# Kernel tuning notes

Measured on AMD Instinct MI355X. Metric: run time of the kernel, lower is better.

Reference implementation:

```python
import jax, jax.numpy as jnp
import numpy as np

B, V, C, H, W, D = 1, 3, 32, 320, 320, 32


def setup_inputs() -> dict:
    key = jax.random.key(0)
    ks = jax.random.split(key, 14)
    feats = jax.random.normal(ks[0], (B, V, C, H, W), jnp.float32)
    # Valid pinhole projections: P = [[K @ [R|t]], [0,0,0,1]], identity rotation,
    # horizontal baselines sized so the warp stays mostly in-image over the depth range.
    K = np.array([[400.0, 0.0, W / 2.0], [0.0, 400.0, H / 2.0], [0.0, 0.0, 1.0]])
    mats = []
    for tx in (0.0, 100.0, -100.0):
        Rt = np.eye(4)
        Rt[0, 3] = tx
        P = np.eye(4)
        P[:3, :4] = K @ Rt[:3, :4]
        mats.append(P)
    proj = jnp.asarray(np.broadcast_to(np.stack(mats)[None], (B, V, 4, 4)).copy(), jnp.float32)
    planes = jnp.linspace(425.0, 935.0, D, dtype=jnp.float32)
    depth_values = jnp.broadcast_to(planes[None, :, None, None], (B, D, H, W)).astype(jnp.float32)
    s = 0.05  # small init so exp(reg_cost) stays well-scaled
    W0 = s * jax.random.normal(ks[1], (8, C, 3, 3), jnp.float32)
    Ws1 = s * jax.random.normal(ks[2], (8, 8, 3, 3), jnp.float32)
    W1 = s * jax.random.normal(ks[3], (16, 8, 3, 3), jnp.float32)
    Ws2 = s * jax.random.normal(ks[4], (16, 16, 3, 3), jnp.float32)
    W2 = s * jax.random.normal(ks[5], (32, 16, 3, 3), jnp.float32)
    Ws3 = s * jax.random.normal(ks[6], (32, 32, 3, 3), jnp.float32)
    W3 = s * jax.random.normal(ks[7], (64, 32, 3, 3), jnp.float32)
    Ws4 = s * jax.random.normal(ks[8], (64, 64, 3, 3), jnp.float32)
    U4 = s * jax.random.normal(ks[9], (32, 64, 1, 1), jnp.float32)
    U3 = s * jax.random.normal(ks[10], (16, 32, 1, 1), jnp.float32)
    U2 = s * jax.random.normal(ks[11], (8, 16, 1, 1), jnp.float32)
    Wout = s * jax.random.normal(ks[12], (1, 8, 3, 3), jnp.float32)
    return dict(feats=feats, proj=proj, depth_values=depth_values, W0=W0, Ws1=Ws1,
                W1=W1, Ws2=Ws2, W2=W2, Ws3=Ws3, W3=W3, Ws4=Ws4, U4=U4, U3=U3, U2=U2, Wout=Wout)


def _conv(x, w, stride=1):
    return jax.lax.conv_general_dilated(x, w, (stride, stride), 'SAME',
                                        dimension_numbers=('NCHW', 'OIHW', 'NCHW'))


def _up2(x):
    return jnp.repeat(jnp.repeat(x, 2, axis=2), 2, axis=3)


def _bilinear(img, x, y):
    # img [C,H,W]; x,y [N] pixel coords; zero padding, align_corners semantics
    Cc, Hh, Ww = img.shape
    x0 = jnp.floor(x)
    y0 = jnp.floor(y)
    wx = x - x0
    wy = y - y0

    def tap(xi, yi):
        valid = ((xi >= 0) & (xi <= Ww - 1) & (yi >= 0) & (yi <= Hh - 1)).astype(img.dtype)
        xc = jnp.clip(xi, 0, Ww - 1).astype(jnp.int32)
        yc = jnp.clip(yi, 0, Hh - 1).astype(jnp.int32)
        return img[:, yc, xc] * valid  # [C,N]

    return (tap(x0, y0) * (1 - wx) * (1 - wy) + tap(x0 + 1, y0) * wx * (1 - wy)
            + tap(x0, y0 + 1) * (1 - wx) * wy + tap(x0 + 1, y0 + 1) * wx * wy)


def _forward(feats, proj, depth_values, W0, Ws1, W1, Ws2, W2, Ws3, W3, Ws4, U4, U3, U2, Wout):
    Bn, Vn, Cn, Hn, Wn = feats.shape
    Dn = depth_values.shape[1]
    N = Hn * Wn
    relu = jax.nn.relu
    ref = feats[:, 0]
    ref_sq = ref * ref
    # Precompute per-src-view rotated pixel rays and translations.
    inv_ref = jnp.linalg.inv(proj[:, 0])                       # [B,4,4]
    rel = jnp.einsum('bvij,bjk->bvik', proj[:, 1:], inv_ref)   # [B,V-1,4,4]
    rot, trans = rel[:, :, :3, :3], rel[:, :, :3, 3]
    ys, xs = jnp.meshgrid(jnp.arange(Hn), jnp.arange(Wn), indexing='ij')
    pix = jnp.stack([xs.ravel(), ys.ravel(), jnp.ones(N)], 0).astype(feats.dtype)  # [3,N]
    rot_pix = jnp.einsum('bvij,jn->bvin', rot, pix)            # [B,V-1,3,N]

    def regularize(x, s1, s2, s3, s4):
        c1 = relu(_conv(x, W0) + _conv(s1, Ws1))
        c2 = relu(_conv(c1, W1, 2) + _conv(s2, Ws2))
        c3 = relu(_conv(c2, W2, 2) + _conv(s3, Ws3))
        c4 = relu(_conv(c3, W3, 2) + _conv(s4, Ws4))
        u3 = c3 + _up2(_conv(c4, U4))
        u2 = c2 + _up2(_conv(u3, U3))
        u1 = c1 + _up2(_conv(u2, U2))
        return _conv(u1, Wout), c1, c2, c3, c4

    def step(carry, depth_slice):  # depth_slice [B,H,W]
        s1, s2, s3, s4, exp_sum, depth_img, max_prob = carry
        vol_sum, vol_sq = ref, ref_sq
        dflat = depth_slice.reshape(Bn, 1, N)
        for v in range(Vn - 1):
            xyz = rot_pix[:, v] * dflat + trans[:, v, :, None]   # [B,3,N]
            px = xyz[:, 0] / xyz[:, 2]
            py = xyz[:, 1] / xyz[:, 2]
            warped = jax.vmap(_bilinear)(feats[:, v + 1], px, py).reshape(Bn, Cn, Hn, Wn)
            vol_sum = vol_sum + warped
            vol_sq = vol_sq + warped * warped
        variance = vol_sq / Vn - (vol_sum / Vn) ** 2
        cost, s1, s2, s3, s4 = regularize(variance, s1, s2, s3, s4)
        prob = jnp.exp(cost)                                     # [B,1,H,W]
        max_prob = jnp.maximum(max_prob, prob)                   # == flag*prob + (1-flag)*max
        depth_img = depth_img + depth_slice[:, None] * prob
        exp_sum = exp_sum + prob
        return (s1, s2, s3, s4, exp_sum, depth_img, max_prob), None

    z = lambda c, h, w: jnp.zeros((Bn, c, h, w), feats.dtype)
    init = (z(8, Hn, Wn), z(16, Hn // 2, Wn // 2), z(32, Hn // 4, Wn // 4), z(64, Hn // 8, Wn // 8),
            z(1, Hn, Wn), z(1, Hn, Wn), z(1, Hn, Wn))
    carry, _ = jax.lax.scan(step, init, jnp.moveaxis(depth_values, 1, 0))
    _, _, _, _, exp_sum, depth_img, max_prob = carry
    es = exp_sum + 1e-10
    depth_map = (depth_img / es)[:, 0]
    prob_map = (max_prob / es)[:, 0]
    return jnp.stack([depth_map, prob_map], axis=1)  # [B,2,H,W]


def reference(feats, proj, depth_values, W0, Ws1, W1, Ws2, W2, Ws3, W3, Ws4, U4, U3, U2, Wout):
    return _forward(feats, proj, depth_values, W0, Ws1, W1, Ws2, W2, Ws3, W3, Ws4, U4, U3, U2, Wout)
```

## Files before the change

### kernel.cpp

```cpp
#include <hip/hip_runtime.h>
#include <hip/hip_bf16.h>
#include <hip/hip_fp16.h>
#include <math.h>

#define HH 320
#define WW 320
#define NP (HH*WW)
#define CC 32
#define DD 32
#define H2 160
#define W2 160
#define N2 (H2*W2)
#define H4 80
#define W4 80
#define N4 (H4*W4)
#define H8 40
#define W8 40
#define N8 (H8*W8)

#define AHW 18
#define AHH 10
#define ANH (AHW*AHH)
#define ABUF_STRIDE 184

#define U3_NPX 24
#define U3_ST  25
#define U2_NPX 60
#define U2_ST  61
#define U1_NPX 180
#define U1_ST  181

#define SMEM_FLOATS (32*U3_ST + 16*U2_ST + 8*U1_ST)

#define C1SZ (8*NP)
#define C2SZ (16*N2)
#define C3SZ (32*N4)
#define C4SZ (64*N8)

#define OFF_REL  0
#define FH_FLOATS (3*CC*NP/2)
#define OFF_FH   64
#define OFF_C1R  (OFF_FH + FH_FLOATS)
#define OFF_C2R  (OFF_C1R + 5*C1SZ)
#define OFF_C3R  (OFF_C2R + 4*C2SZ)
#define OFF_C4R  (OFF_C3R + 3*C3SZ)
#define OFF_ESUM (OFF_C4R + 2*C4SZ)
#define OFF_DIMG (OFF_ESUM + NP)
#define OFF_MAXP (OFF_DIMG + NP)
#define OFF_END  (OFF_MAXP + NP)

#define D_BEG 0
#define C_BEG 128
#define B_BEG 352
#define A_BEG 752
#define U_BEG 1552
#define TOT_BLK 2352

__global__ void k_prep(const float* __restrict__ proj, float* __restrict__ rel) {
    if (threadIdx.x != 0 || blockIdx.x != 0) return;
    double a[4][8];
    for (int i = 0; i < 4; i++)
        for (int j = 0; j < 4; j++) {
            a[i][j] = (double)proj[i*4 + j];
            a[i][j+4] = (i == j) ? 1.0 : 0.0;
        }
    for (int c = 0; c < 4; c++) {
        int pv = c; double best = fabs(a[c][c]);
        for (int r = c+1; r < 4; r++) {
            double v = fabs(a[r][c]);
            if (v > best) { best = v; pv = r; }
        }
        if (pv != c)
            for (int j = 0; j < 8; j++) { double t = a[c][j]; a[c][j] = a[pv][j]; a[pv][j] = t; }
        double inv = 1.0 / a[c][c];
        for (int j = 0; j < 8; j++) a[c][j] *= inv;
        for (int r = 0; r < 4; r++) if (r != c) {
            double f = a[r][c];
            for (int j = 0; j < 8; j++) a[r][j] -= f * a[c][j];
        }
    }
    for (int v = 1; v < 3; v++) {
        const float* P = proj + v*16;
        double rm[4][4];
        for (int i = 0; i < 4; i++)
            for (int j = 0; j < 4; j++) {
                double s = 0.0;
                for (int k = 0; k < 4; k++) s += (double)P[i*4 + k] * a[k][j+4];
                rm[i][j] = s;
            }
        float* o = rel + (v-1)*12;
        o[0]=(float)rm[0][0]; o[1]=(float)rm[0][1]; o[2]=(float)rm[0][2];
        o[3]=(float)rm[1][0]; o[4]=(float)rm[1][1]; o[5]=(float)rm[1][2];
        o[6]=(float)rm[2][0]; o[7]=(float)rm[2][1]; o[8]=(float)rm[2][2];
        o[9]=(float)rm[0][3]; o[10]=(float)rm[1][3]; o[11]=(float)rm[2][3];
    }
}

__global__ __launch_bounds__(256) void k_tofp16(const float* __restrict__ feats,
                                                __half* __restrict__ fh) {
    int i = blockIdx.x*256 + threadIdx.x;
    int base = i*8;
    if (base >= 3*CC*NP) return;
    float4 a = *(const float4*)(feats + base);
    float4 b = *(const float4*)(feats + base + 4);
    __half h[8];
    h[0]=__float2half(a.x); h[1]=__float2half(a.y); h[2]=__float2half(a.z); h[3]=__float2half(a.w);
    h[4]=__float2half(b.x); h[5]=__float2half(b.y); h[6]=__float2half(b.z); h[7]=__float2half(b.w);
    *(float4*)(fh + base) = *(float4*)h;
}


__device__ void stageA(int blk, int d,
        const __half* __restrict__ fh, const float* __restrict__ rel,
        const float* __restrict__ depthv, float* __restrict__ c1r,
        const float* __restrict__ W0, const float* __restrict__ Ws1,
        float* buf) {
    const float* s1 = c1r + (size_t)((d+4)%5)*C1SZ;
    float* c1out = c1r + (size_t)(d%5)*C1SZ;
    int bx = blk % 20, by = blk / 20;
    int ox0 = bx*16, oy0 = by*8;
    int tid = threadIdx.x;

    int ppix[2]; bool inimg[2];
    int rb[2][4];
    float cf[2][8];
#pragma unroll
    for (int j = 0; j < 2; j++) {
        int hp = tid + j*128;
        inimg[j] = false; ppix[j] = 0;
#pragma unroll
        for (int q = 0; q < 4; q++) rb[j][q] = 0;
#pragma unroll
        for (int q = 0; q < 8; q++) cf[j][q] = 0.0f;
        if (hp < ANH) {
            int hy = hp / AHW, hx = hp - hy*AHW;
            int gy = oy0 + hy - 1, gx = ox0 + hx - 1;
            if (gy >= 0 && gy < HH && gx >= 0 && gx < WW) {
                inimg[j] = true;
                int p = gy*WW + gx; ppix[j] = p;
                float depth = depthv[(size_t)d*NP + p];
                float fx = (float)gx, fy = (float)gy;
#pragma unroll
                for (int v = 0; v < 2; v++) {
                    const float* r = rel + v*12;
                    float X = (r[0]*fx + r[1]*fy + r[2]) * depth + r[9];
                    float Y = (r[3]*fx + r[4]*fy + r[5]) * depth + r[10];
                    float Z = (r[6]*fx + r[7]*fy + r[8]) * depth + r[11];
                    float iz = 1.0f / Z;
                    float px = fminf(fmaxf(X*iz, -2.0f), (float)(WW+1));
                    float py = fminf(fmaxf(Y*iz, -2.0f), (float)(HH+1));
                    float x0f = floorf(px), y0f = floorf(py);
                    float wx = px - x0f, wy = py - y0f;
                    int x0 = (int)x0f, y0 = (int)y0f;
                    int xb = min(max(x0, 0), WW-2);
                    float cA, cB;
                    if (x0 >= 0 && x0 <= WW-2)      { cA = 1.0f-wx; cB = wx; }
                    else if (x0 == -1)              { cA = wx;      cB = 0.0f; }
                    else if (x0 == WW-1)            { cA = 0.0f;    cB = 1.0f-wx; }
                    else                            { cA = 0.0f;    cB = 0.0f; }
#pragma unroll
                    for (int rr = 0; rr < 2; rr++) {
                        int yr = y0 + rr;
                        float wyr = rr ? wy : 1.0f-wy;
                        bool vy = (yr >= 0) && (yr < HH);
                        int yrc = min(max(yr, 0), HH-1);
                        rb[j][v*2+rr] = yrc*WW + xb;
                        cf[j][v*4+rr*2+0] = vy ? wyr*cA : 0.0f;
                        cf[j][v*4+rr*2+1] = vy ? wyr*cB : 0.0f;
                    }
                }
            }
        }
    }

    int opx = tid & 15, opy = tid >> 4;
    float acc[8];
#pragma unroll
    for (int o = 0; o < 8; o++) acc[o] = 0.0f;
    const float inv3 = 1.0f/3.0f;

    for (int chunk = 0; chunk < 4; chunk++) {
        int c0 = chunk*8;
#pragma unroll
        for (int j = 0; j < 2; j++) {
            int hp = tid + j*128;
            if (hp < ANH) {
                if (!inimg[j]) {
#pragma unroll
                    for (int c = 0; c < 8; c++) buf[c*ABUF_STRIDE + hp] = 0.0f;
                } else {
                    int p = ppix[j];
#pragma unroll
                    for (int c = 0; c < 8; c++) {
                        int cg = c0 + c;
                        float rv = __half2float(fh[(size_t)cg*NP + p]);
                        const __half* p1 = fh + (size_t)(CC + cg)*NP;
                        float t1 = cf[j][0]*__half2float(p1[rb[j][0]])
                                 + cf[j][1]*__half2float(p1[rb[j][0]+1])
                                 + cf[j][2]*__half2float(p1[rb[j][1]])
                                 + cf[j][3]*__half2float(p1[rb[j][1]+1]);
                        const __half* p2 = fh + (size_t)(2*CC + cg)*NP;
                        float t2 = cf[j][4]*__half2float(p2[rb[j][2]])
                                 + cf[j][5]*__half2float(p2[rb[j][2]+1])
                                 + cf[j][6]*__half2float(p2[rb[j][3]])
                                 + cf[j][7]*__half2float(p2[rb[j][3]+1]);
                        float sum = rv + t1 + t2;
                        float sq  = rv*rv + t1*t1 + t2*t2;
                        float m = sum*inv3;
                        buf[c*ABUF_STRIDE + hp] = sq*inv3 - m*m;
                    }
                }
            }
        }
        __syncthreads();
        for (int ci = 0; ci < 8; ci++) {
            float t[9];
#pragma unroll
            for (int ky = 0; ky < 3; ky++)
#pragma unroll
                for (int kx = 0; kx < 3; kx++)
                    t[ky*3+kx] = buf[ci*ABUF_STRIDE + (opy+ky)*AHW + opx + kx];
#pragma unroll
            for (int o = 0; o < 8; o++) {
                const float* w = W0 + (o*32 + c0 + ci)*9;
                float a = acc[o];
#pragma unroll
                for (int k = 0; k < 9; k++) a += t[k]*w[k];
                acc[o] = a;
            }
        }
        __syncthreads();
    }

#pragma unroll
    for (int j = 0; j < 2; j++) {
        int hp = tid + j*128;
        if (hp < ANH) {
#pragma unroll
            for (int c = 0; c < 8; c++)
                buf[c*ABUF_STRIDE + hp] = inimg[j] ? s1[(size_t)c*NP + ppix[j]] : 0.0f;
        }
    }
    __syncthreads();
    for (int ci = 0; ci < 8; ci++) {
        float t[9];
#pragma unroll
        for (int ky = 0; ky < 3; ky++)
#pragma unroll
            for (int kx = 0; kx < 3; kx++)
                t[ky*3+kx] = buf[ci*ABUF_STRIDE + (opy+ky)*AHW + opx + kx];
#pragma unroll
        for (int o = 0; o < 8; o++) {
            const float* w = Ws1 + (o*8 + ci)*9;
            float a = acc[o];
#pragma unroll
            for (int k = 0; k < 9; k++) a += t[k]*w[k];
            acc[o] = a;
        }
    }
    int outp = (oy0 + opy)*WW + ox0 + opx;
#pragma unroll
    for (int o = 0; o < 8; o++) c1out[(size_t)o*NP + outp] = fmaxf(acc[o], 0.0f);
}

__device__ void stageB(int chunk, int og, int d,
        const float* __restrict__ c1r, float* __restrict__ c2r,
        const float* __restrict__ W1, const float* __restrict__ Ws2) {
    const float* c1 = c1r + (size_t)(d%5)*C1SZ;
    const float* s2 = c2r + (size_t)((d+3)%4)*C2SZ;
    float* c2 = c2r + (size_t)(d%4)*C2SZ;
    int p = chunk*128 + threadIdx.x;
    int y = p / W2, x = p - y*W2;
    int offsA[9]; float mskA[9];
#pragma unroll
    for (int k = 0; k < 9; k++) {
        int yy = 2*y + k/3, xx = 2*x + k%3;
        bool v = (yy < HH) && (xx < WW);
        offsA[k] = v ? yy*WW + xx : 0;
        mskA[k] = v ? 1.0f : 0.0f;
    }
    int offsB[9]; float mskB[9];
#pragma unroll
    for (int k = 0; k < 9; k++) {
        int yy = y + k/3 - 1, xx = x + k%3 - 1;
        bool v = (yy >= 0) && (yy < H2) && (xx >= 0) && (xx < W2);
        offsB[k] = v ? yy*W2 + xx : 0;
        mskB[k] = v ? 1.0f : 0.0f;
    }
    float acc[8];
#pragma unroll
    for (int o = 0; o < 8; o++) acc[o] = 0.0f;
    for (int ci = 0; ci < 8; ci++) {
        const float* b = c1 + (size_t)ci*NP;
        float t[9];
#pragma unroll
        for (int k = 0; k < 9; k++) t[k] = b[offsA[k]] * mskA[k];
#pragma unroll
        for (int o = 0; o < 8; o++) {
            const float* w = W1 + ((og*8 + o)*8 + ci)*9;
            float a = acc[o];
#pragma unroll
            for (int k = 0; k < 9; k++) a += t[k]*w[k];
            acc[o] = a;
        }
    }
    for (int ci = 0; ci < 16; ci++) {
        const float* b = s2 + (size_t)ci*N2;
        float t[9];
#pragma unroll
        for (int k = 0; k < 9; k++) t[k] = b[offsB[k]] * mskB[k];
#pragma unroll
        for (int o = 0; o < 8; o++) {
            const float* w = Ws2 + ((og*8 + o)*16 + ci)*9;
            float a = acc[o];
#pragma unroll
            for (int k = 0; k < 9; k++) a += t[k]*w[k];
            acc[o] = a;
        }
    }
#pragma unroll
    for (int o = 0; o < 8; o++) c2[(size_t)(og*8 + o)*N2 + p] = fmaxf(acc[o], 0.0f);
}

__device__ void stageC(int chunk, int og, int d,
        const float* __restrict__ c2r, float* __restrict__ c3r,
        const float* __restrict__ W2w, const float* __restrict__ Ws3) {
    const float* c2 = c2r + (size_t)(d%4)*C2SZ;
    const float* s3 = c3r + (size_t)((d+2)%3)*C3SZ;
    float* c3 = c3r + (size_t)(d%3)*C3SZ;
    int p = chunk*128 + threadIdx.x;
    int y = p / W4, x = p - y*W4;
    int offsA[9]; float mskA[9];
#pragma unroll
    for (int k = 0; k < 9; k++) {
        int yy = 2*y + k/3, xx = 2*x + k%3;
        bool v = (yy < H2) && (xx < W2);
        offsA[k] = v ? yy*W2 + xx : 0;
        mskA[k] = v ? 1.0f : 0.0f;
    }
    int offsB[9]; float mskB[9];
#pragma unroll
    for (int k = 0; k < 9; k++) {
        int yy = y + k/3 - 1, xx = x + k%3 - 1;
        bool v = (yy >= 0) && (yy < H4) && (xx >= 0) && (xx < W4);
        offsB[k] = v ? yy*W4 + xx : 0;
        mskB[k] = v ? 1.0f : 0.0f;
    }
    float acc[8];
#pragma unroll
    for (int o = 0; o < 8; o++) acc[o] = 0.0f;
    for (int ci = 0; ci < 16; ci++) {
        const float* b = c2 + (size_t)ci*N2;
        float t[9];
#pragma unroll
        for (int k = 0; k < 9; k++) t[k] = b[offsA[k]] * mskA[k];
#pragma unroll
        for (int o = 0; o < 8; o++) {
            const float* w = W2w + ((og*8 + o)*16 + ci)*9;
            float a = acc[o];
#pragma unroll
            for (int k = 0; k < 9; k++) a += t[k]*w[k];
            acc[o] = a;
        }
    }
    for (int ci = 0; ci < 32; ci++) {
        const float* b = s3 + (size_t)ci*N4;
        float t[9];
#pragma unroll
        for (int k = 0; k < 9; k++) t[k] = b[offsB[k]] * mskB[k];
#pragma unroll
        for (int o = 0; o < 8; o++) {
            const float* w = Ws3 + ((og*8 + o)*32 + ci)*9;
            float a = acc[o];
#pragma unroll
            for (int k = 0; k < 9; k++) a += t[k]*w[k];
            acc[o] = a;
        }
    }
#pragma unroll
    for (int o = 0; o < 8; o++) c3[(size_t)(og*8 + o)*N4 + p] = fmaxf(acc[o], 0.0f);
}

__device__ void stageD(int chunk, int og, int d,
        const float* __restrict__ c3r, float* __restrict__ c4r,
        const float* __restrict__ W3w, const float* __restrict__ Ws4) {
    const float* c3 = c3r + (size_t)(d%3)*C3SZ;
    const float* s4 = c4r + (size_t)((d+1)%2)*C4SZ;
    float* c4 = c4r + (size_t)(d%2)*C4SZ;
    int p = chunk*128 + threadIdx.x;
    if (p >= N8) return;
    int y = p / W8, x = p - y*W8;
    int offsA[9]; float mskA[9];
#pragma unroll
    for (int k = 0; k < 9; k++) {
        int yy = 2*y + k/3, xx = 2*x + k%3;
        bool v = (yy < H4) && (xx < W4);
        offsA[k] = v ? yy*W4 + xx : 0;
        mskA[k] = v ? 1.0f : 0.0f;
    }
    int offsB[9]; float mskB[9];
#pragma unroll
    for (int k = 0; k < 9; k++) {
        int yy = y + k/3 - 1, xx = x + k%3 - 1;
        bool v = (yy >= 0) && (yy < H8) && (xx >= 0) && (xx < W8);
        offsB[k] = v ? yy*W8 + xx : 0;
        mskB[k] = v ? 1.0f : 0.0f;
    }
    float acc[8];
#pragma unroll
    for (int o = 0; o < 8; o++) acc[o] = 0.0f;
    for (int ci = 0; ci < 32; ci++) {
        const float* b = c3 + (size_t)ci*N4;
        float t[9];
#pragma unroll
        for (int k = 0; k < 9; k++) t[k] = b[offsA[k]] * mskA[k];
#pragma unroll
        for (int o = 0; o < 8; o++) {
            const float* w = W3w + ((og*8 + o)*32 + ci)*9;
            float a = acc[o];
#pragma unroll
            for (int k = 0; k < 9; k++) a += t[k]*w[k];
            acc[o] = a;
        }
    }
    for (int ci = 0; ci < 64; ci++) {
        const float* b = s4 + (size_t)ci*N8;
        float t[9];
#pragma unroll
        for (int k = 0; k < 9; k++) t[k] = b[offsB[k]] * mskB[k];
#pragma unroll
        for (int o = 0; o < 8; o++) {
            const float* w = Ws4 + ((og*8 + o)*64 + ci)*9;
            float a = acc[o];
#pragma unroll
            for (int k = 0; k < 9; k++) a += t[k]*w[k];
            acc[o] = a;
        }
    }
#pragma unroll
    for (int o = 0; o < 8; o++) c4[(size_t)(og*8 + o)*N8 + p] = fmaxf(acc[o], 0.0f);
}

__device__ void stageU(int blk, int d,
        const float* __restrict__ c1r, const float* __restrict__ c2r,
        const float* __restrict__ c3r, const float* __restrict__ c4r,
        const float* __restrict__ U4, const float* __restrict__ U3w,
        const float* __restrict__ U2w, const float* __restrict__ Wout,
        const float* __restrict__ depthv,
        float* __restrict__ esum, float* __restrict__ dimg,
        float* __restrict__ maxp, float* smem) {
    const float* c1 = c1r + (size_t)(d%5)*C1SZ;
    const float* c2 = c2r + (size_t)(d%4)*C2SZ;
    const float* c3 = c3r + (size_t)(d%3)*C3SZ;
    const float* c4 = c4r + (size_t)(d%2)*C4SZ;
    const float* dsl = depthv + (size_t)d*NP;
    float* u3s = smem;
    float* u2s = smem + 32*U3_ST;
    float* u1s = u2s + 16*U2_ST;
    int bx = blk % 20, by = blk / 20;
    int x0 = bx*16, y0 = by*8;
    int qx0 = (x0>>2) - 1, qy0 = (y0>>2) - 1;
    int hx0 = (x0>>1) - 1, hy0 = (y0>>1) - 1;
    int tid = threadIdx.x;

    for (int i = tid; i < 32*U3_NPX; i += 128) {
        int ch = i / U3_NPX, pp = i - ch*U3_NPX;
        int y4 = qy0 + pp/6, x4 = qx0 + pp%6;
        int y4c = min(max(y4,0),H4-1), x4c = min(max(x4,0),W4-1);
        int pl = (y4c>>1)*W8 + (x4c>>1);
        const float* w = U4 + ch*64;
        float s = c3[(size_t)ch*N4 + y4c*W4 + x4c];
#pragma unroll 8
        for (int ci = 0; ci < 64; ci++) s += c4[(size_t)ci*N8 + pl]*w[ci];
        u3s[ch*U3_ST + pp] = s;
    }
    __syncthreads();
    for (int i = tid; i < 16*U2_NPX; i += 128) {
        int ch = i / U2_NPX, pp = i - ch*U2_NPX;
        int y2 = hy0 + pp/10, x2 = hx0 + pp%10;
        int y2c = min(max(y2,0),H2-1), x2c = min(max(x2,0),W2-1);
        int ly = (y2c>>1)-qy0, lx = (x2c>>1)-qx0;
        const float* w = U3w + ch*32;
        float s = c2[(size_t)ch*N2 + y2c*W2 + x2c];
#pragma unroll 8
        for (int ci = 0; ci < 32; ci++) s += u3s[ci*U3_ST + ly*6 + lx]*w[ci];
        u2s[ch*U2_ST + pp] = s;
    }
    __syncthreads();
    for (int i = tid; i < 8*U1_NPX; i += 128) {
        int ch = i / U1_NPX, pp = i - ch*U1_NPX;
        int gy = y0 + pp/AHW - 1, gx = x0 + pp%AHW - 1;
        float s = 0.0f;
        if (gy >= 0 && gy < HH && gx >= 0 && gx < WW) {
            int ly = (gy>>1)-hy0, lx = (gx>>1)-hx0;
            const float* w = U2w + ch*16;
            s = c1[(size_t)ch*NP + gy*WW + gx];
#pragma unroll
            for (int ci = 0; ci < 16; ci++) s += u2s[ci*U2_ST + ly*10 + lx]*w[ci];
        }
        u1s[ch*U1_ST + pp] = s;
    }
    __syncthreads();
    int opx = tid & 15, opy = tid >> 4;
    int base = opy*AHW + opx;
    float cost = 0.0f;
#pragma unroll
    for (int ci = 0; ci < 8; ci++) {
        const float* w = Wout + ci*9;
#pragma unroll
        for (int ky = 0; ky < 3; ky++)
#pragma unroll
            for (int kx = 0; kx < 3; kx++)
                cost += u1s[ci*U1_ST + base + ky*AHW + kx]*w[ky*3+kx];
    }
    int p = (y0+opy)*WW + x0 + opx;
    float prob = expf(cost);
    esum[p] += prob;
    dimg[p] += dsl[p]*prob;
    maxp[p] = fmaxf(maxp[p], prob);
}

__global__ __launch_bounds__(128) void k_uber(
        int t,
        const __half* __restrict__ fh, const float* __restrict__ rel,
        const float* __restrict__ depthv,
        const float* __restrict__ W0, const float* __restrict__ Ws1,
        const float* __restrict__ W1, const float* __restrict__ Ws2,
        const float* __restrict__ W2w, const float* __restrict__ Ws3,
        const float* __restrict__ W3w, const float* __restrict__ Ws4,
        const float* __restrict__ U4, const float* __restrict__ U3,
        const float* __restrict__ U2, const float* __restrict__ Wout,
        float* __restrict__ c1r, float* __restrict__ c2r,
        float* __restrict__ c3r, float* __restrict__ c4r,
        float* __restrict__ esum, float* __restrict__ dimg,
        float* __restrict__ maxp) {
    __shared__ float smem[SMEM_FLOATS];
    int b = blockIdx.x;
    if (b < C_BEG) {
        int d = t - 3;
        int og = b / 16, chunk = b % 16;
        if (d >= 0 && d < DD && chunk < 13) stageD(chunk, og, d, c3r, c4r, W3w, Ws4);
    } else if (b < B_BEG) {
        int d = t - 2;
        int local = b - C_BEG;
        int og = local / 56, chunk = local % 56;
        if (d >= 0 && d < DD && chunk < 50) stageC(chunk, og, d, c2r, c3r, W2w, Ws3);
    } else if (b < A_BEG) {
        int d = t - 1;
        int local = b - B_BEG;
        int og = local / 200, chunk = local % 200;
        if (d >= 0 && d < DD) stageB(chunk, og, d, c1r, c2r, W1, Ws2);
    } else if (b < U_BEG) {
        int d = t;
        if (d < DD) stageA(b - A_BEG, d, fh, rel, depthv, c1r, W0, Ws1, smem);
    } else {
        int d = t - 4;
        if (d >= 0 && d < DD)
            stageU(b - U_BEG, d, c1r, c2r, c3r, c4r, U4, U3, U2, Wout, depthv,
                   esum, dimg, maxp, smem);
    }
}

__global__ __launch_bounds__(256) void k_final(
        const float* __restrict__ exp_sum, const float* __restrict__ depth_img,
        const float* __restrict__ max_prob, float* __restrict__ out) {
    int p = blockIdx.x*256 + threadIdx.x;
    if (p >= NP) return;
    float es = exp_sum[p] + 1e-10f;
    out[p] = depth_img[p] / es;
    out[NP + p] = max_prob[p] / es;
}

extern "C" void kernel_launch(void* const* d_in, const int* in_sizes, int n_in,
                              void* d_out, int out_size, void* d_ws, size_t ws_size,
                              hipStream_t stream) {
    const float* feats = (const float*)d_in[0];
    const float* proj  = (const float*)d_in[1];
    const float* depthv= (const float*)d_in[2];
    const float* W0  = (const float*)d_in[3];
    const float* Ws1 = (const float*)d_in[4];
    const float* W1  = (const float*)d_in[5];
    const float* Ws2 = (const float*)d_in[6];
    const float* W2w = (const float*)d_in[7];
    const float* Ws3 = (const float*)d_in[8];
    const float* W3w = (const float*)d_in[9];
    const float* Ws4 = (const float*)d_in[10];
    const float* U4  = (const float*)d_in[11];
    const float* U3  = (const float*)d_in[12];
    const float* U2  = (const float*)d_in[13];
    const float* Wout= (const float*)d_in[14];

    float* ws = (float*)d_ws;
    float* rel  = ws + OFF_REL;
    __half* fh  = (__half*)(ws + OFF_FH);
    float* c1r  = ws + OFF_C1R;
    float* c2r  = ws + OFF_C2R;
    float* c3r  = ws + OFF_C3R;
    float* c4r  = ws + OFF_C4R;
    float* esum = ws + OFF_ESUM;
    float* dimg = ws + OFF_DIMG;
    float* maxp = ws + OFF_MAXP;

    hipMemsetAsync(c1r, 0, (size_t)(OFF_END - OFF_C1R) * sizeof(float), stream);
    k_prep<<<1, 1, 0, stream>>>(proj, rel);
    k_tofp16<<<dim3(3*CC*NP/8/256), 256, 0, stream>>>(feats, fh);

    for (int t = 0; t < DD + 4; t++) {
        k_uber<<<dim3(TOT_BLK), 128, 0, stream>>>(t, fh, rel, depthv,
            W0, Ws1, W1, Ws2, W2w, Ws3, W3w, Ws4, U4, U3, U2, Wout,
            c1r, c2r, c3r, c4r, esum, dimg, maxp);
    }
    k_final<<<dim3(400), 256, 0, stream>>>(esum, dimg, maxp, (float*)d_out);
}
```

Baseline: 3.125 ms.

## Switch fp16 features to pixel-major layout and double uber-kernel block size

The fp16 feature copy now uses a channel-last layout with 32 halves per pixel. Stage A's bilinear gathers become 16-byte vector loads of 8 channels instead of scalar strided half loads, and stage A splits its 8 output channels across two 128-thread halves. Blocks are raised to 256 threads: stages B/C/D cover 256 pixels per block and stage U covers a 16x16 tile, so block counts per stage are recomputed. This aims to cut gather transactions and the number of blocks. The cost is a strided transpose in the conversion kernel and more shared memory per block.

```diff
diff --git a/kernel.cpp b/kernel.cpp
--- a/kernel.cpp
+++ b/kernel.cpp
@@ -19,18 +19,13 @@
 #define N8 (H8*W8)
 
 #define AHW 18
-#define AHH 10
-#define ANH (AHW*AHH)
+#define ANH (AHW*10)
 #define ABUF_STRIDE 184
 
-#define U3_NPX 24
-#define U3_ST  25
-#define U2_NPX 60
-#define U2_ST  61
-#define U1_NPX 180
-#define U1_ST  181
-
-#define SMEM_FLOATS (32*U3_ST + 16*U2_ST + 8*U1_ST)
+#define U3S 37
+#define U2S 101
+#define U1S 325
+#define SMEM_FLOATS (32*U3S + 16*U2S + 8*U1S)
 
 #define C1SZ (8*NP)
 #define C2SZ (16*N2)
@@ -38,7 +33,7 @@
 #define C4SZ (64*N8)
 
 #define OFF_REL  0
-#define FH_FLOATS (3*CC*NP/2)
+#define FH_FLOATS (3*NP*CC/2)
 #define OFF_FH   64
 #define OFF_C1R  (OFF_FH + FH_FLOATS)
 #define OFF_C2R  (OFF_C1R + 5*C1SZ)
@@ -50,11 +45,18 @@
 #define OFF_END  (OFF_MAXP + NP)
 
 #define D_BEG 0
-#define C_BEG 128
-#define B_BEG 352
-#define A_BEG 752
-#define U_BEG 1552
-#define TOT_BLK 2352
+#define C_BEG 64
+#define B_BEG 192
+#define A_BEG 400
+#define U_BEG 1200
+#define TOT_BLK 1600
+
+__device__ __forceinline__ void load8h(const __half* b, float o[8]) {
+    float4 f = *reinterpret_cast<const float4*>(b);
+    const __half2* h = reinterpret_cast<const __half2*>(&f);
+#pragma unroll
+    for (int j = 0; j < 4; j++) { float2 t = __half22float2(h[j]); o[2*j] = t.x; o[2*j+1] = t.y; }
+}
 
 __global__ void k_prep(const float* __restrict__ proj, float* __restrict__ rel) {
     if (threadIdx.x != 0 || blockIdx.x != 0) return;
@@ -99,14 +101,15 @@
 __global__ __launch_bounds__(256) void k_tofp16(const float* __restrict__ feats,
                                                 __half* __restrict__ fh) {
     int i = blockIdx.x*256 + threadIdx.x;
-    int base = i*8;
-    if (base >= 3*CC*NP) return;
-    float4 a = *(const float4*)(feats + base);
-    float4 b = *(const float4*)(feats + base + 4);
-    __half h[8];
-    h[0]=__float2half(a.x); h[1]=__float2half(a.y); h[2]=__float2half(a.z); h[3]=__float2half(a.w);
-    h[4]=__float2half(b.x); h[5]=__float2half(b.y); h[6]=__float2half(b.z); h[7]=__float2half(b.w);
-    *(float4*)(fh + base) = *(float4*)h;
+    if (i >= 3*NP) return;
+    int v = i / NP, p = i - v*NP;
+    const float* src = feats + (size_t)v*CC*NP + p;
+    union { __half h[32]; float4 f4[4]; } u;
+#pragma unroll
+    for (int c = 0; c < 32; c++) u.h[c] = __float2half(src[(size_t)c*NP]);
+    float4* dst = (float4*)(fh + (size_t)i*32);
+#pragma unroll
+    for (int q = 0; q < 4; q++) dst[q] = u.f4[q];
 }
 
 
@@ -121,94 +124,87 @@
     int ox0 = bx*16, oy0 = by*8;
     int tid = threadIdx.x;
 
-    int ppix[2]; bool inimg[2];
-    int rb[2][4];
-    float cf[2][8];
-#pragma unroll
-    for (int j = 0; j < 2; j++) {
-        int hp = tid + j*128;
-        inimg[j] = false; ppix[j] = 0;
-#pragma unroll
-        for (int q = 0; q < 4; q++) rb[j][q] = 0;
-#pragma unroll
-        for (int q = 0; q < 8; q++) cf[j][q] = 0.0f;
-        if (hp < ANH) {
-            int hy = hp / AHW, hx = hp - hy*AHW;
-            int gy = oy0 + hy - 1, gx = ox0 + hx - 1;
-            if (gy >= 0 && gy < HH && gx >= 0 && gx < WW) {
-                inimg[j] = true;
-                int p = gy*WW + gx; ppix[j] = p;
-                float depth = depthv[(size_t)d*NP + p];
-                float fx = (float)gx, fy = (float)gy;
-#pragma unroll
-                for (int v = 0; v < 2; v++) {
-                    const float* r = rel + v*12;
-                    float X = (r[0]*fx + r[1]*fy + r[2]) * depth + r[9];
-                    float Y = (r[3]*fx + r[4]*fy + r[5]) * depth + r[10];
-                    float Z = (r[6]*fx + r[7]*fy + r[8]) * depth + r[11];
-                    float iz = 1.0f / Z;
-                    float px = fminf(fmaxf(X*iz, -2.0f), (float)(WW+1));
-                    float py = fminf(fmaxf(Y*iz, -2.0f), (float)(HH+1));
-                    float x0f = floorf(px), y0f = floorf(py);
-                    float wx = px - x0f, wy = py - y0f;
-                    int x0 = (int)x0f, y0 = (int)y0f;
-                    int xb = min(max(x0, 0), WW-2);
-                    float cA, cB;
-                    if (x0 >= 0 && x0 <= WW-2)      { cA = 1.0f-wx; cB = wx; }
-                    else if (x0 == -1)              { cA = wx;      cB = 0.0f; }
-                    else if (x0 == WW-1)            { cA = 0.0f;    cB = 1.0f-wx; }
-                    else                            { cA = 0.0f;    cB = 0.0f; }
-#pragma unroll
-                    for (int rr = 0; rr < 2; rr++) {
-                        int yr = y0 + rr;
-                        float wyr = rr ? wy : 1.0f-wy;
-                        bool vy = (yr >= 0) && (yr < HH);
-                        int yrc = min(max(yr, 0), HH-1);
-                        rb[j][v*2+rr] = yrc*WW + xb;
-                        cf[j][v*4+rr*2+0] = vy ? wyr*cA : 0.0f;
-                        cf[j][v*4+rr*2+1] = vy ? wyr*cB : 0.0f;
-                    }
+    int ppix = 0; bool inimg = false;
+    int rb[4]; float cf[8];
+#pragma unroll
+    for (int q = 0; q < 4; q++) rb[q] = 0;
+#pragma unroll
+    for (int q = 0; q < 8; q++) cf[q] = 0.0f;
+    if (tid < ANH) {
+        int hy = tid / AHW, hx = tid - hy*AHW;
+        int gy = oy0 + hy - 1, gx = ox0 + hx - 1;
+        if (gy >= 0 && gy < HH && gx >= 0 && gx < WW) {
+            inimg = true;
+            int p = gy*WW + gx; ppix = p;
+            float depth = depthv[(size_t)d*NP + p];
+            float fx = (float)gx, fy = (float)gy;
+#pragma unroll
+            for (int v = 0; v < 2; v++) {
+                const float* r = rel + v*12;
+                float X = (r[0]*fx + r[1]*fy + r[2]) * depth + r[9];
+                float Y = (r[3]*fx + r[4]*fy + r[5]) * depth + r[10];
+                float Z = (r[6]*fx + r[7]*fy + r[8]) * depth + r[11];
+                float iz = 1.0f / Z;
+                float px = fminf(fmaxf(X*iz, -2.0f), (float)(WW+1));
+                float py = fminf(fmaxf(Y*iz, -2.0f), (float)(HH+1));
+                float x0f = floorf(px), y0f = floorf(py);
+                float wx = px - x0f, wy = py - y0f;
+                int x0 = (int)x0f, y0 = (int)y0f;
+                int xb = min(max(x0, 0), WW-2);
+                float cA, cB;
+                if (x0 >= 0 && x0 <= WW-2)      { cA = 1.0f-wx; cB = wx; }
+                else if (x0 == -1)              { cA = wx;      cB = 0.0f; }
+                else if (x0 == WW-1)            { cA = 0.0f;    cB = 1.0f-wx; }
+                else                            { cA = 0.0f;    cB = 0.0f; }
+#pragma unroll
+                for (int rr = 0; rr < 2; rr++) {
+                    int yr = y0 + rr;
+                    float wyr = rr ? wy : 1.0f-wy;
+                    bool vy = (yr >= 0) && (yr < HH);
+                    int yrc = min(max(yr, 0), HH-1);
+                    rb[v*2+rr] = yrc*WW + xb;
+                    cf[v*4+rr*2+0] = vy ? wyr*cA : 0.0f;
+                    cf[v*4+rr*2+1] = vy ? wyr*cB : 0.0f;
                 }
             }
         }
     }
 
-    int opx = tid & 15, opy = tid >> 4;
-    float acc[8];
-#pragma unroll
-    for (int o = 0; o < 8; o++) acc[o] = 0.0f;
+    int spx = tid & 127;
+    int opx = spx & 15, opy = spx >> 4;
+    int ob = (tid >> 7) * 4;
+    float acc[4] = {0.0f, 0.0f, 0.0f, 0.0f};
     const float inv3 = 1.0f/3.0f;
+    const __half* f1 = fh + (size_t)NP*32;
+    const __half* f2 = fh + (size_t)2*NP*32;
 
     for (int chunk = 0; chunk < 4; chunk++) {
         int c0 = chunk*8;
-#pragma unroll
-        for (int j = 0; j < 2; j++) {
-            int hp = tid + j*128;
-            if (hp < ANH) {
-                if (!inimg[j]) {
-#pragma unroll
-                    for (int c = 0; c < 8; c++) buf[c*ABUF_STRIDE + hp] = 0.0f;
-                } else {
-                    int p = ppix[j];
-#pragma unroll
-                    for (int c = 0; c < 8; c++) {
-                        int cg = c0 + c;
-                        float rv = __half2float(fh[(size_t)cg*NP + p]);
-                        const __half* p1 = fh + (size_t)(CC + cg)*NP;
-                        float t1 = cf[j][0]*__half2float(p1[rb[j][0]])
-                                 + cf[j][1]*__half2float(p1[rb[j][0]+1])
-                                 + cf[j][2]*__half2float(p1[rb[j][1]])
-                                 + cf[j][3]*__half2float(p1[rb[j][1]+1]);
-                        const __half* p2 = fh + (size_t)(2*CC + cg)*NP;
-                        float t2 = cf[j][4]*__half2float(p2[rb[j][2]])
-                                 + cf[j][5]*__half2float(p2[rb[j][2]+1])
-                                 + cf[j][6]*__half2float(p2[rb[j][3]])
-                                 + cf[j][7]*__half2float(p2[rb[j][3]+1]);
-                        float sum = rv + t1 + t2;
-                        float sq  = rv*rv + t1*t1 + t2*t2;
-                        float m = sum*inv3;
-                        buf[c*ABUF_STRIDE + hp] = sq*inv3 - m*m;
-                    }
+        if (tid < ANH) {
+            if (!inimg) {
+#pragma unroll
+                for (int c = 0; c < 8; c++) buf[c*ABUF_STRIDE + tid] = 0.0f;
+            } else {
+                float r8[8]; load8h(fh + (size_t)ppix*32 + c0, r8);
+                float a0[8], a1[8], a2[8], a3[8];
+                load8h(f1 + (size_t)rb[0]*32 + c0, a0);
+                load8h(f1 + (size_t)(rb[0]+1)*32 + c0, a1);
+                load8h(f1 + (size_t)rb[1]*32 + c0, a2);
+                load8h(f1 + (size_t)(rb[1]+1)*32 + c0, a3);
+                float b0[8], b1[8], b2[8], b3[8];
+                load8h(f2 + (size_t)rb[2]*32 + c0, b0);
+                load8h(f2 + (size_t)(rb[2]+1)*32 + c0, b1);
+                load8h(f2 + (size_t)rb[3]*32 + c0, b2);
+                load8h(f2 + (size_t)(rb[3]+1)*32 + c0, b3);
+#pragma unroll
+                for (int c = 0; c < 8; c++) {
+                    float t1 = cf[0]*a0[c] + cf[1]*a1[c] + cf[2]*a2[c] + cf[3]*a3[c];
+                    float t2 = cf[4]*b0[c] + cf[5]*b1[c] + cf[6]*b2[c] + cf[7]*b3[c];
+                    float rv = r8[c];
+                    float sum = rv + t1 + t2;
+                    float sq  = rv*rv + t1*t1 + t2*t2;
+                    float m = sum*inv3;
+                    buf[c*ABUF_STRIDE + tid] = sq*inv3 - m*m;
                 }
             }
         }
@@ -221,8 +217,8 @@
                 for (int kx = 0; kx < 3; kx++)
                     t[ky*3+kx] = buf[ci*ABUF_STRIDE + (opy+ky)*AHW + opx + kx];
 #pragma unroll
-            for (int o = 0; o < 8; o++) {
-                const float* w = W0 + (o*32 + c0 + ci)*9;
+            for (int o = 0; o < 4; o++) {
+                const float* w = W0 + ((ob+o)*32 + c0 + ci)*9;
                 float a = acc[o];
 #pragma unroll
                 for (int k = 0; k < 9; k++) a += t[k]*w[k];
@@ -232,14 +228,10 @@
         __syncthreads();
     }
 
-#pragma unroll
-    for (int j = 0; j < 2; j++) {
-        int hp = tid + j*128;
-        if (hp < ANH) {
-#pragma unroll
-            for (int c = 0; c < 8; c++)
-                buf[c*ABUF_STRIDE + hp] = inimg[j] ? s1[(size_t)c*NP + ppix[j]] : 0.0f;
-        }
+    if (tid < ANH) {
+#pragma unroll
+        for (int c = 0; c < 8; c++)
+            buf[c*ABUF_STRIDE + tid] = inimg ? s1[(size_t)c*NP + ppix] : 0.0f;
     }
     __syncthreads();
     for (int ci = 0; ci < 8; ci++) {
@@ -250,8 +242,8 @@
             for (int kx = 0; kx < 3; kx++)
                 t[ky*3+kx] = buf[ci*ABUF_STRIDE + (opy+ky)*AHW + opx + kx];
 #pragma unroll
-        for (int o = 0; o < 8; o++) {
-            const float* w = Ws1 + (o*8 + ci)*9;
+        for (int o = 0; o < 4; o++) {
+            const float* w = Ws1 + ((ob+o)*8 + ci)*9;
             float a = acc[o];
 #pragma unroll
             for (int k = 0; k < 9; k++) a += t[k]*w[k];
@@ -260,7 +252,7 @@
     }
     int outp = (oy0 + opy)*WW + ox0 + opx;
 #pragma unroll
-    for (int o = 0; o < 8; o++) c1out[(size_t)o*NP + outp] = fmaxf(acc[o], 0.0f);
+    for (int o = 0; o < 4; o++) c1out[(size_t)(ob+o)*NP + outp] = fmaxf(acc[o], 0.0f);
 }
 
 __device__ void stageB(int chunk, int og, int d,
@@ -269,7 +261,7 @@
     const float* c1 = c1r + (size_t)(d%5)*C1SZ;
     const float* s2 = c2r + (size_t)((d+3)%4)*C2SZ;
     float* c2 = c2r + (size_t)(d%4)*C2SZ;
-    int p = chunk*128 + threadIdx.x;
+    int p = chunk*256 + threadIdx.x;
     int y = p / W2, x = p - y*W2;
     int offsA[9]; float mskA[9];
 #pragma unroll
@@ -328,7 +320,7 @@
     const float* c2 = c2r + (size_t)(d%4)*C2SZ;
     const float* s3 = c3r + (size_t)((d+2)%3)*C3SZ;
     float* c3 = c3r + (size_t)(d%3)*C3SZ;
-    int p = chunk*128 + threadIdx.x;
+    int p = chunk*256 + threadIdx.x;
     int y = p / W4, x = p - y*W4;
     int offsA[9]; float mskA[9];
 #pragma unroll
@@ -387,7 +379,7 @@
     const float* c3 = c3r + (size_t)(d%3)*C3SZ;
     const float* s4 = c4r + (size_t)((d+1)%2)*C4SZ;
     float* c4 = c4r + (size_t)(d%2)*C4SZ;
-    int p = chunk*128 + threadIdx.x;
+    int p = chunk*256 + threadIdx.x;
     if (p >= N8) return;
     int y = p / W8, x = p - y*W8;
     int offsA[9]; float mskA[9];
@@ -455,16 +447,16 @@
     const float* c4 = c4r + (size_t)(d%2)*C4SZ;
     const float* dsl = depthv + (size_t)d*NP;
     float* u3s = smem;
-    float* u2s = smem + 32*U3_ST;
-    float* u1s = u2s + 16*U2_ST;
+    float* u2s = smem + 32*U3S;
+    float* u1s = u2s + 16*U2S;
     int bx = blk % 20, by = blk / 20;
-    int x0 = bx*16, y0 = by*8;
+    int x0 = bx*16, y0 = by*16;
     int qx0 = (x0>>2) - 1, qy0 = (y0>>2) - 1;
     int hx0 = (x0>>1) - 1, hy0 = (y0>>1) - 1;
     int tid = threadIdx.x;
 
-    for (int i = tid; i < 32*U3_NPX; i += 128) {
-        int ch = i / U3_NPX, pp = i - ch*U3_NPX;
+    for (int i = tid; i < 32*36; i += 256) {
+        int ch = i / 36, pp = i - ch*36;
         int y4 = qy0 + pp/6, x4 = qx0 + pp%6;
         int y4c = min(max(y4,0),H4-1), x4c = min(max(x4,0),W4-1);
         int pl = (y4c>>1)*W8 + (x4c>>1);
@@ -472,37 +464,37 @@
         float s = c3[(size_t)ch*N4 + y4c*W4 + x4c];
 #pragma unroll 8
         for (int ci = 0; ci < 64; ci++) s += c4[(size_t)ci*N8 + pl]*w[ci];
-        u3s[ch*U3_ST + pp] = s;
+        u3s[ch*U3S + pp] = s;
     }
     __syncthreads();
-    for (int i = tid; i < 16*U2_NPX; i += 128) {
-        int ch = i / U2_NPX, pp = i - ch*U2_NPX;
+    for (int i = tid; i < 16*100; i += 256) {
+        int ch = i / 100, pp = i - ch*100;
         int y2 = hy0 + pp/10, x2 = hx0 + pp%10;
         int y2c = min(max(y2,0),H2-1), x2c = min(max(x2,0),W2-1);
         int ly = (y2c>>1)-qy0, lx = (x2c>>1)-qx0;
         const float* w = U3w + ch*32;
         float s = c2[(size_t)ch*N2 + y2c*W2 + x2c];
 #pragma unroll 8
-        for (int ci = 0; ci < 32; ci++) s += u3s[ci*U3_ST + ly*6 + lx]*w[ci];
-        u2s[ch*U2_ST + pp] = s;
+        for (int ci = 0; ci < 32; ci++) s += u3s[ci*U3S + ly*6 + lx]*w[ci];
+        u2s[ch*U2S + pp] = s;
     }
     __syncthreads();
-    for (int i = tid; i < 8*U1_NPX; i += 128) {
-        int ch = i / U1_NPX, pp = i - ch*U1_NPX;
-        int gy = y0 + pp/AHW - 1, gx = x0 + pp%AHW - 1;
+    for (int i = tid; i < 8*324; i += 256) {
+        int ch = i / 324, pp = i - ch*324;
+        int gy = y0 + pp/18 - 1, gx = x0 + pp%18 - 1;
         float s = 0.0f;
         if (gy >= 0 && gy < HH && gx >= 0 && gx < WW) {
             int ly = (gy>>1)-hy0, lx = (gx>>1)-hx0;
             const float* w = U2w + ch*16;
             s = c1[(size_t)ch*NP + gy*WW + gx];
 #pragma unroll
-            for (int ci = 0; ci < 16; ci++) s += u2s[ci*U2_ST + ly*10 + lx]*w[ci];
-        }
-        u1s[ch*U1_ST + pp] = s;
+            for (int ci = 0; ci < 16; ci++) s += u2s[ci*U2S + ly*10 + lx]*w[ci];
+        }
+        u1s[ch*U1S + pp] = s;
     }
     __syncthreads();
     int opx = tid & 15, opy = tid >> 4;
-    int base = opy*AHW + opx;
+    int base = opy*18 + opx;
     float cost = 0.0f;
 #pragma unroll
     for (int ci = 0; ci < 8; ci++) {
@@ -511,7 +503,7 @@
         for (int ky = 0; ky < 3; ky++)
 #pragma unroll
             for (int kx = 0; kx < 3; kx++)
-                cost += u1s[ci*U1_ST + base + ky*AHW + kx]*w[ky*3+kx];
+                cost += u1s[ci*U1S + base + ky*18 + kx]*w[ky*3+kx];
     }
     int p = (y0+opy)*WW + x0 + opx;
     float prob = expf(cost);
@@ -520,7 +512,7 @@
     maxp[p] = fmaxf(maxp[p], prob);
 }
 
-__global__ __launch_bounds__(128) void k_uber(
+__global__ __launch_bounds__(256) void k_uber(
         int t,
         const __half* __restrict__ fh, const float* __restrict__ rel,
         const float* __restrict__ depthv,
@@ -538,18 +530,18 @@
     int b = blockIdx.x;
     if (b < C_BEG) {
         int d = t - 3;
-        int og = b / 16, chunk = b % 16;
-        if (d >= 0 && d < DD && chunk < 13) stageD(chunk, og, d, c3r, c4r, W3w, Ws4);
+        int og = b / 8, chunk = b % 8;
+        if (d >= 0 && d < DD && chunk < 7) stageD(chunk, og, d, c3r, c4r, W3w, Ws4);
     } else if (b < B_BEG) {
         int d = t - 2;
         int local = b - C_BEG;
-        int og = local / 56, chunk = local % 56;
-        if (d >= 0 && d < DD && chunk < 50) stageC(chunk, og, d, c2r, c3r, W2w, Ws3);
+        int og = local / 32, chunk = local % 32;
+        if (d >= 0 && d < DD && chunk < 25) stageC(chunk, og, d, c2r, c3r, W2w, Ws3);
     } else if (b < A_BEG) {
         int d = t - 1;
         int local = b - B_BEG;
-        int og = local / 200, chunk = local % 200;
-        if (d >= 0 && d < DD) stageB(chunk, og, d, c1r, c2r, W1, Ws2);
+        int og = local / 104, chunk = local % 104;
+        if (d >= 0 && d < DD && chunk < 100) stageB(chunk, og, d, c1r, c2r, W1, Ws2);
     } else if (b < U_BEG) {
         int d = t;
         if (d < DD) stageA(b - A_BEG, d, fh, rel, depthv, c1r, W0, Ws1, smem);
@@ -603,10 +595,10 @@
 
     hipMemsetAsync(c1r, 0, (size_t)(OFF_END - OFF_C1R) * sizeof(float), stream);
     k_prep<<<1, 1, 0, stream>>>(proj, rel);
-    k_tofp16<<<dim3(3*CC*NP/8/256), 256, 0, stream>>>(feats, fh);
+    k_tofp16<<<dim3((3*NP + 255)/256), 256, 0, stream>>>(feats, fh);
 
     for (int t = 0; t < DD + 4; t++) {
-        k_uber<<<dim3(TOT_BLK), 128, 0, stream>>>(t, fh, rel, depthv,
+        k_uber<<<dim3(TOT_BLK), 256, 0, stream>>>(t, fh, rel, depthv,
             W0, Ws1, W1, Ws2, W2w, Ws3, W3w, Ws4, U4, U3, U2, Wout,
             c1r, c2r, c3r, c4r, esum, dimg, maxp);
     }
```

Measured after the change: 3.357 ms. 1.07x slower.
